# Kernel tuning notes

Hardware: AMD Instinct MI355X
Metric: run time of the kernel (lower is better)

## Reference

```python
import jax, jax.numpy as jnp
import numpy as np

B, S, HID, H, DK = 16, 1024, 512, 8, 64
NEG = -1e30


def setup_inputs() -> dict:
    key = jax.random.key(0)
    kx, kl, kq, kk, kv, ko = jax.random.split(key, 6)
    x = jax.random.normal(kx, (B, S, HID), dtype=jnp.float32)
    # mask is a prefix of ones per sample (the torch code fills nmask[i, :nsum, :nsum])
    lengths = jax.random.randint(kl, (B,), S // 2, S + 1)
    mask = (jnp.arange(S)[None, :] < lengths[:, None]).astype(jnp.int32)
    scale = 0.02
    Wq = jax.random.normal(kq, (H, HID, DK), dtype=jnp.float32) * scale  # stacked per-head Linear weights
    Wk = jax.random.normal(kk, (H, HID, DK), dtype=jnp.float32) * scale
    Wv = jax.random.normal(kv, (H, HID, DK), dtype=jnp.float32) * scale
    Wout = jax.random.normal(ko, (H * DK, HID), dtype=jnp.float32) * scale
    return {"x": x, "mask": mask, "Wq": Wq, "Wk": Wk, "Wv": Wv, "Wout": Wout}


def reference(x, mask, Wq, Wk, Wv, Wout):
    # x: [B,S,HID], mask: [B,S] int prefix mask
    nsum = mask.sum(-1).astype(jnp.float32)          # [B]
    valid = mask.astype(bool)                         # [B,S]
    pair = valid[:, :, None] & valid[:, None, :]      # [B,S,S] == nmask from the torch loop
    # batched per-head projections (equivalent to the per-head Linear loop)
    Q = jnp.einsum('bsh,nhd->bnsd', x, Wq)            # [B,H,S,DK]
    K = jnp.einsum('bsh,nhd->bnsd', x, Wk)
    V = jnp.einsum('bsh,nhd->bnsd', x, Wv)
    scores = jnp.einsum('bnqd,bnkd->bnqk', Q, K)      # [B,H,S,S]
    scores = scores / jnp.sqrt(nsum)[:, None, None, None]  # per-sample sqrt(len) scale
    scores = jnp.where(pair[:, None, :, :], scores, NEG)   # masked_softmax: -1e30 at masked slots
    p = jax.nn.softmax(scores, axis=-1)
    attn = jnp.einsum('bnqk,bnkd->bnqd', p, V)        # [B,H,S,DK]
    h = attn.transpose(0, 2, 1, 3).reshape(B, S, H * DK)  # concat heads along feature dim
    return jnp.einsum('bsf,fh->bsh', h, Wout)         # W_out, no bias
```

## Files before the change

kernel.cpp:

```cpp
#include <hip/hip_runtime.h>
#include <math.h>

constexpr int CB = 16;
constexpr int CS = 1024;
constexpr int CHID = 512;
constexpr int CH = 8;
constexpr int CDK = 64;

typedef _Float16 f16;
typedef __attribute__((ext_vector_type(8))) _Float16 f16x8;
typedef __attribute__((ext_vector_type(4))) _Float16 f16x4;
typedef __attribute__((ext_vector_type(4))) float f32x4;

__device__ inline f32x4 mfma16(f16x8 a, f16x8 b, f32x4 c) {
  return __builtin_amdgcn_mfma_f32_16x16x32_f16(a, b, c, 0, 0, 0);
}

__global__ __launch_bounds__(256) void lengths_kernel(const int* __restrict__ mask,
                                                      int* __restrict__ lens,
                                                      float* __restrict__ Vsum) {
  const int b = blockIdx.x, t = threadIdx.x;
  const int g = b * 256 + t;
  Vsum[g * 2] = 0.f;
  Vsum[g * 2 + 1] = 0.f;
  __shared__ int red[256];
  int s = 0;
  for (int i = t; i < CS; i += 256) s += mask[b * CS + i];
  red[t] = s;
  __syncthreads();
  for (int off = 128; off > 0; off >>= 1) {
    if (t < off) red[t] += red[t + off];
    __syncthreads();
  }
  if (t == 0) lens[b] = red[0];
}

__global__ __launch_bounds__(256) void cast_x_kernel(const float4* __restrict__ x,
                                                     f16x4* __restrict__ xh) {
  const int idx = blockIdx.x * 256 + threadIdx.x;
  const float4 v = x[idx];
  f16x4 o;
  o[0] = (f16)v.x; o[1] = (f16)v.y; o[2] = (f16)v.z; o[3] = (f16)v.w;
  xh[idx] = o;
}

__global__ __launch_bounds__(256) void cast_w_kernel(const float* __restrict__ Wq,
                                                     const float* __restrict__ Wk,
                                                     const float* __restrict__ Wv,
                                                     const float* __restrict__ Wout,
                                                     f16* __restrict__ wtAll) {
  const int y = blockIdx.y, kb = blockIdx.x, t = threadIdx.x;
  const int k0 = kb * 64;
  const float* src;
  int ldsrc;
  f16* dst;
  if (y < 24) {
    const int which = y >> 3, h = y & 7;
    const float* W = (which == 0) ? Wq : (which == 1) ? Wk : Wv;
    src = W + (size_t)h * 32768 + (size_t)k0 * 64;
    ldsrc = 64;
    dst = wtAll + (size_t)which * 262144 + (size_t)h * 32768;
  } else {
    const int c = y - 24;
    src = Wout + (size_t)k0 * 512 + c * 64;
    ldsrc = 512;
    dst = wtAll + (size_t)3 * 262144 + (size_t)c * 64 * 512;
  }

  __shared__ float Ts[64][68];
  {
    const int kr = t >> 4, cg = (t & 15) * 4;
#pragma unroll
    for (int rr = 0; rr < 4; ++rr) {
      const float4 v = *(const float4*)&src[(size_t)(rr * 16 + kr) * ldsrc + cg];
      Ts[rr * 16 + kr][cg] = v.x;
      Ts[rr * 16 + kr][cg + 1] = v.y;
      Ts[rr * 16 + kr][cg + 2] = v.z;
      Ts[rr * 16 + kr][cg + 3] = v.w;
    }
  }
  __syncthreads();
  {
    const int n = t >> 2, seg = t & 3;
    f16x8 a, b;
#pragma unroll
    for (int j = 0; j < 8; ++j) {
      a[j] = (f16)Ts[seg * 16 + j][n];
      b[j] = (f16)Ts[seg * 16 + 8 + j][n];
    }
    f16* d = &dst[(size_t)n * 512 + k0 + seg * 16];
    *(f16x8*)d = a;
    *(f16x8*)(d + 8) = b;
  }
}

__global__ __launch_bounds__(256) void qkvf_kernel(
    const f16* __restrict__ xh, const f16* __restrict__ wtAll,
    const int* __restrict__ lens, f16* __restrict__ Qh, f16* __restrict__ Kh,
    f16* __restrict__ Vth, float* __restrict__ Vsum) {
  const int rt = blockIdx.x, ct = blockIdx.y;
  const int which = ct >> 2, hp = ct & 3;
  const f16* Wt = wtAll + (size_t)which * 262144 + (size_t)hp * 65536;
  const int row0 = rt * 128;
  const int b = row0 >> 10, s0 = row0 & 1023;
  const int h0 = hp * 2;
  const int t = threadIdx.x;
  const int w = t >> 6, lane = t & 63, quad = lane >> 4, lcol = lane & 15;
  const int wr = w >> 1, wc = w & 1;

  __shared__ union SM {
    struct { f16 Xs[128][40]; f16 Ws[128][40]; } a;
    f16 Ts[128][136];
  } sm;

  f32x4 acc[4][4];
#pragma unroll
  for (int i = 0; i < 4; ++i)
#pragma unroll
    for (int j = 0; j < 4; ++j) acc[i][j] = (f32x4){0.f, 0.f, 0.f, 0.f};

  f16x8 px[2], pw[2];
#pragma unroll
  for (int i = 0; i < 2; ++i) {
    const int c = t + 256 * i, r = c >> 2, sg = c & 3;
    px[i] = *(const f16x8*)&xh[(size_t)(row0 + r) * CHID + sg * 8];
    pw[i] = *(const f16x8*)&Wt[(size_t)r * CHID + sg * 8];
  }

  for (int k0 = 0; k0 < CHID; k0 += 32) {
    __syncthreads();
#pragma unroll
    for (int i = 0; i < 2; ++i) {
      const int c = t + 256 * i, r = c >> 2, sg = c & 3;
      *(f16x8*)&sm.a.Xs[r][sg * 8] = px[i];
      *(f16x8*)&sm.a.Ws[r][sg * 8] = pw[i];
    }
    __syncthreads();
    const int kn = (k0 + 32 < CHID) ? k0 + 32 : k0;
#pragma unroll
    for (int i = 0; i < 2; ++i) {
      const int c = t + 256 * i, r = c >> 2, sg = c & 3;
      px[i] = *(const f16x8*)&xh[(size_t)(row0 + r) * CHID + kn + sg * 8];
      pw[i] = *(const f16x8*)&Wt[(size_t)r * CHID + kn + sg * 8];
    }
    f16x8 af[4], bf[4];
#pragma unroll
    for (int i = 0; i < 4; ++i)
      af[i] = *(const f16x8*)&sm.a.Xs[wr * 64 + i * 16 + lcol][quad * 8];
#pragma unroll
    for (int j = 0; j < 4; ++j)
      bf[j] = *(const f16x8*)&sm.a.Ws[wc * 64 + j * 16 + lcol][quad * 8];
#pragma unroll
    for (int i = 0; i < 4; ++i)
#pragma unroll
      for (int j = 0; j < 4; ++j) acc[i][j] = mfma16(af[i], bf[j], acc[i][j]);
  }

  if (which == 2) {
#pragma unroll
    for (int j = 0; j < 4; ++j) {
      float ps = 0.f;
#pragma unroll
      for (int i = 0; i < 4; ++i)
#pragma unroll
        for (int rr = 0; rr < 4; ++rr) ps += acc[i][j][rr];
      ps += __shfl_xor(ps, 16);
      ps += __shfl_xor(ps, 32);
      if (quad == 0) {
        const int d128 = wc * 64 + j * 16 + lcol;
        const int h = h0 + (d128 >> 6), d = d128 & 63;
        atomicAdd(&Vsum[((size_t)b * CH + h) * CDK + d], ps);
      }
    }
    __syncthreads();
#pragma unroll
    for (int i = 0; i < 4; ++i)
#pragma unroll
      for (int j = 0; j < 4; ++j)
#pragma unroll
        for (int rr = 0; rr < 4; ++rr)
          sm.Ts[wc * 64 + j * 16 + lcol][wr * 64 + i * 16 + quad * 4 + rr] =
              (f16)acc[i][j][rr];
    __syncthreads();
    const int nl = t >> 1, half = t & 1;
    const int h = h0 + (nl >> 6), d = nl & 63;
    f16* dst = &Vth[(((size_t)b * CH + h) * CDK + d) * CS + s0 + half * 64];
#pragma unroll
    for (int c8 = 0; c8 < 8; ++c8)
      *(f16x8*)&dst[c8 * 8] = *(const f16x8*)&sm.Ts[nl][half * 64 + c8 * 8];
  } else {
    f16* O = (which == 0) ? Qh : Kh;
    const float qsc = (which == 0) ? rsqrtf((float)lens[b]) : 1.0f;
    const int h = h0 + wc;
#pragma unroll
    for (int i = 0; i < 4; ++i) {
#pragma unroll
      for (int rr = 0; rr < 4; ++rr) {
        const int s = s0 + wr * 64 + i * 16 + quad * 4 + rr;
        const size_t base = (((size_t)b * CH + h) * CS + s) * CDK;
#pragma unroll
        for (int j = 0; j < 4; ++j)
          O[base + j * 16 + lcol] = (f16)(acc[i][j][rr] * qsc);
      }
    }
  }
}

__global__ __launch_bounds__(256) void attn_kernel(
    const f16* __restrict__ Qh, const f16* __restrict__ Kh,
    const f16* __restrict__ Vth, const int* __restrict__ lens,
    const float* __restrict__ Vsum, f16* __restrict__ Hbh) {
  const int qt = blockIdx.x, h = blockIdx.y, b = blockIdx.z;
  const int n = lens[b];
  const int nt = (n + 63) >> 6;
  const int t = threadIdx.x, w = t >> 6, lane = t & 63, quad = lane >> 4,
            lcol = lane & 15;

  __shared__ f16 Ks[64][72];
  __shared__ f16 Vs[64][72];
  __shared__ f16 Pt[4][32][72];

  const size_t bh = ((size_t)b * CH + h) * CS;
  const size_t bhd = ((size_t)b * CH + h) * CDK;

  const int qbase = qt * 128 + w * 32;
  f16x8 qa[2][2];
#pragma unroll
  for (int set = 0; set < 2; ++set) {
    const size_t qr = bh + qbase + set * 16 + lcol;
    qa[set][0] = *(const f16x8*)&Qh[qr * CDK + quad * 8];
    qa[set][1] = *(const f16x8*)&Qh[qr * CDK + 32 + quad * 8];
  }

  f32x4 o[2][4];
#pragma unroll
  for (int set = 0; set < 2; ++set)
#pragma unroll
    for (int dt = 0; dt < 4; ++dt) o[set][dt] = (f32x4){0.f, 0.f, 0.f, 0.f};
  float lp[2][4] = {{0.f, 0.f, 0.f, 0.f}, {0.f, 0.f, 0.f, 0.f}};

  f16x8 pk[2], pv[2];
#pragma unroll
  for (int i = 0; i < 2; ++i) {
    const int c = t + 256 * i, r = c >> 3, sg = c & 7;
    pk[i] = *(const f16x8*)&Kh[(bh + r) * CDK + sg * 8];
    pv[i] = *(const f16x8*)&Vth[(bhd + r) * CS + sg * 8];
  }

  for (int kt = 0; kt < nt; ++kt) {
    __syncthreads();
#pragma unroll
    for (int i = 0; i < 2; ++i) {
      const int c = t + 256 * i, r = c >> 3, sg = c & 7;
      *(f16x8*)&Ks[r][sg * 8] = pk[i];
      *(f16x8*)&Vs[r][sg * 8] = pv[i];
    }
    __syncthreads();
    const int ktn = (kt + 1 < nt) ? kt + 1 : kt;
#pragma unroll
    for (int i = 0; i < 2; ++i) {
      const int c = t + 256 * i, r = c >> 3, sg = c & 7;
      pk[i] = *(const f16x8*)&Kh[(bh + ktn * 64 + r) * CDK + sg * 8];
      pv[i] = *(const f16x8*)&Vth[(bhd + r) * CS + ktn * 64 + sg * 8];
    }

#pragma unroll
    for (int set = 0; set < 2; ++set) {
      f32x4 st[4];
#pragma unroll
      for (int ct = 0; ct < 4; ++ct) {
        const f16x8 kb0 = *(const f16x8*)&Ks[ct * 16 + lcol][quad * 8];
        const f16x8 kb1 = *(const f16x8*)&Ks[ct * 16 + lcol][32 + quad * 8];
        st[ct] = mfma16(qa[set][0], kb0, (f32x4){0.f, 0.f, 0.f, 0.f});
        st[ct] = mfma16(qa[set][1], kb1, st[ct]);
      }
#pragma unroll
      for (int ct = 0; ct < 4; ++ct) {
        const bool kvld = (kt * 64 + ct * 16 + lcol) < n;
#pragma unroll
        for (int r = 0; r < 4; ++r) {
          float p = __expf(st[ct][r]);
          p = kvld ? p : 0.f;
          lp[set][r] += p;
          Pt[w][set * 16 + quad * 4 + r][ct * 16 + lcol] = (f16)p;
        }
      }
    }

    f16x8 pa[2][2];
#pragma unroll
    for (int set = 0; set < 2; ++set) {
      pa[set][0] = *(const f16x8*)&Pt[w][set * 16 + lcol][quad * 8];
      pa[set][1] = *(const f16x8*)&Pt[w][set * 16 + lcol][32 + quad * 8];
    }

#pragma unroll
    for (int dt = 0; dt < 4; ++dt) {
      const f16x8 vb0 = *(const f16x8*)&Vs[dt * 16 + lcol][quad * 8];
      const f16x8 vb1 = *(const f16x8*)&Vs[dt * 16 + lcol][32 + quad * 8];
#pragma unroll
      for (int set = 0; set < 2; ++set) {
        o[set][dt] = mfma16(pa[set][0], vb0, o[set][dt]);
        o[set][dt] = mfma16(pa[set][1], vb1, o[set][dt]);
      }
    }
  }

  float invl[2][4];
#pragma unroll
  for (int set = 0; set < 2; ++set)
#pragma unroll
    for (int r = 0; r < 4; ++r) {
      float v = lp[set][r];
      v += __shfl_xor(v, 1);
      v += __shfl_xor(v, 2);
      v += __shfl_xor(v, 4);
      v += __shfl_xor(v, 8);
      invl[set][r] = 1.0f / v;
    }

#pragma unroll
  for (int set = 0; set < 2; ++set)
#pragma unroll
    for (int dt = 0; dt < 4; ++dt)
#pragma unroll
      for (int r = 0; r < 4; ++r) {
        const int srow = qbase + set * 16 + quad * 4 + r;
        const int d = dt * 16 + lcol;
        const float val = (srow < n) ? o[set][dt][r] * invl[set][r]
                                     : Vsum[bhd + d] * (1.0f / 1024.0f);
        Hbh[((size_t)b * CS + srow) * (CH * CDK) + h * CDK + d] = (f16)val;
      }
}

__global__ __launch_bounds__(256) void outp_kernel(const f16* __restrict__ Hbh,
                                                   const f16* __restrict__ woutt,
                                                   float* __restrict__ out) {
  const int rt = blockIdx.x, ctile = blockIdx.y;
  const int row0 = rt * 128, col0 = ctile * 128;
  const f16* Wt = woutt + (size_t)col0 * CHID;
  const int t = threadIdx.x;
  const int w = t >> 6, lane = t & 63, quad = lane >> 4, lcol = lane & 15;
  const int wr = w >> 1, wc = w & 1;

  __shared__ f16 Hs[128][40];
  __shared__ f16 Ws[128][40];

  f32x4 acc[4][4];
#pragma unroll
  for (int i = 0; i < 4; ++i)
#pragma unroll
    for (int j = 0; j < 4; ++j) acc[i][j] = (f32x4){0.f, 0.f, 0.f, 0.f};

  f16x8 ph[2], pw[2];
#pragma unroll
  for (int i = 0; i < 2; ++i) {
    const int c = t + 256 * i, r = c >> 2, sg = c & 3;
    ph[i] = *(const f16x8*)&Hbh[(size_t)(row0 + r) * CHID + sg * 8];
    pw[i] = *(const f16x8*)&Wt[(size_t)r * CHID + sg * 8];
  }

  for (int k0 = 0; k0 < CHID; k0 += 32) {
    __syncthreads();
#pragma unroll
    for (int i = 0; i < 2; ++i) {
      const int c = t + 256 * i, r = c >> 2, sg = c & 3;
      *(f16x8*)&Hs[r][sg * 8] = ph[i];
      *(f16x8*)&Ws[r][sg * 8] = pw[i];
    }
    __syncthreads();
    const int kn = (k0 + 32 < CHID) ? k0 + 32 : k0;
#pragma unroll
    for (int i = 0; i < 2; ++i) {
      const int c = t + 256 * i, r = c >> 2, sg = c & 3;
      ph[i] = *(const f16x8*)&Hbh[(size_t)(row0 + r) * CHID + kn + sg * 8];
      pw[i] = *(const f16x8*)&Wt[(size_t)r * CHID + kn + sg * 8];
    }
    f16x8 af[4], bf[4];
#pragma unroll
    for (int i = 0; i < 4; ++i)
      af[i] = *(const f16x8*)&Hs[wr * 64 + i * 16 + lcol][quad * 8];
#pragma unroll
    for (int j = 0; j < 4; ++j)
      bf[j] = *(const f16x8*)&Ws[wc * 64 + j * 16 + lcol][quad * 8];
#pragma unroll
    for (int i = 0; i < 4; ++i)
#pragma unroll
      for (int j = 0; j < 4; ++j) acc[i][j] = mfma16(af[i], bf[j], acc[i][j]);
  }

#pragma unroll
  for (int i = 0; i < 4; ++i) {
#pragma unroll
    for (int rr = 0; rr < 4; ++rr) {
      const size_t rg = row0 + wr * 64 + i * 16 + quad * 4 + rr;
#pragma unroll
      for (int j = 0; j < 4; ++j)
        out[rg * CHID + col0 + wc * 64 + j * 16 + lcol] = acc[i][j][rr];
    }
  }
}

extern "C" void kernel_launch(void* const* d_in, const int* in_sizes, int n_in,
                              void* d_out, int out_size, void* d_ws,
                              size_t ws_size, hipStream_t stream) {
  const float* x = (const float*)d_in[0];
  const int* mask = (const int*)d_in[1];
  const float* Wq = (const float*)d_in[2];
  const float* Wk = (const float*)d_in[3];
  const float* Wv = (const float*)d_in[4];
  const float* Wout = (const float*)d_in[5];
  float* out = (float*)d_out;

  char* ws = (char*)d_ws;
  int* lens = (int*)ws;
  size_t off = 1024;
  const size_t NX = (size_t)CB * CS * CHID;
  const size_t NW = (size_t)CH * CHID * CDK;
  f16* xh = (f16*)(ws + off);    off += NX * 2;
  f16* wtAll = (f16*)(ws + off); off += NW * 4 * 2;
  f16* Qh = (f16*)(ws + off);    off += NX * 2;
  f16* Kh = (f16*)(ws + off);    off += NX * 2;
  f16* Vth = (f16*)(ws + off);   off += NX * 2;
  f16* Hbh = (f16*)(ws + off);   off += NX * 2;
  float* Vsum = (float*)(ws + off); off += (size_t)CB * CH * CDK * 4;
  f16* woutt = wtAll + NW * 3;

  lengths_kernel<<<CB, 256, 0, stream>>>(mask, lens, Vsum);
  cast_x_kernel<<<NX / 4 / 256, 256, 0, stream>>>((const float4*)x, (f16x4*)xh);
  cast_w_kernel<<<dim3(8, 32), 256, 0, stream>>>(Wq, Wk, Wv, Wout, wtAll);
  qkvf_kernel<<<dim3(128, 12), 256, 0, stream>>>(xh, wtAll, lens, Qh, Kh, Vth,
                                                 Vsum);
  attn_kernel<<<dim3(CS / 128, CH, CB), 256, 0, stream>>>(Qh, Kh, Vth, lens,
                                                          Vsum, Hbh);
  outp_kernel<<<dim3(128, 4), 256, 0, stream>>>(Hbh, woutt, out);
}
```

Before: 213.5 us.

## Fuse prep kernels, coalesce stores via LDS, skip fully masked query tiles

Merges the length-reduction and x-cast kernels into one launch, and swaps the qkvf grid order so blocks sharing an x row tile run together. Q/K and attention-output stores are staged through shared memory and written as 16-byte vectors instead of scattered scalar stores. Attention blocks whose whole query tile lies past the valid length now write the mean-V fill directly and return early. The log2(e) factor is folded into the Q scale so the kernel can use exp2f, and K fragments are loaded once per tile instead of once per row set. The extra LDS staging adds barriers and some shared-memory traffic.

```diff
diff --git a/kernel.cpp b/kernel.cpp
--- a/kernel.cpp
+++ b/kernel.cpp
@@ -16,32 +16,36 @@
   return __builtin_amdgcn_mfma_f32_16x16x32_f16(a, b, c, 0, 0, 0);
 }
 
-__global__ __launch_bounds__(256) void lengths_kernel(const int* __restrict__ mask,
-                                                      int* __restrict__ lens,
-                                                      float* __restrict__ Vsum) {
-  const int b = blockIdx.x, t = threadIdx.x;
-  const int g = b * 256 + t;
-  Vsum[g * 2] = 0.f;
-  Vsum[g * 2 + 1] = 0.f;
+#define LOG2E 1.4426950408889634f
+
+__global__ __launch_bounds__(256) void prep_kernel(const float4* __restrict__ x,
+                                                   f16x4* __restrict__ xh,
+                                                   const int* __restrict__ mask,
+                                                   int* __restrict__ lens,
+                                                   float* __restrict__ Vsum) {
+  const int bid = blockIdx.x, t = threadIdx.x;
   __shared__ int red[256];
-  int s = 0;
-  for (int i = t; i < CS; i += 256) s += mask[b * CS + i];
-  red[t] = s;
-  __syncthreads();
-  for (int off = 128; off > 0; off >>= 1) {
-    if (t < off) red[t] += red[t + off];
-    __syncthreads();
-  }
-  if (t == 0) lens[b] = red[0];
-}
-
-__global__ __launch_bounds__(256) void cast_x_kernel(const float4* __restrict__ x,
-                                                     f16x4* __restrict__ xh) {
-  const int idx = blockIdx.x * 256 + threadIdx.x;
-  const float4 v = x[idx];
-  f16x4 o;
-  o[0] = (f16)v.x; o[1] = (f16)v.y; o[2] = (f16)v.z; o[3] = (f16)v.w;
-  xh[idx] = o;
+  if (bid < 8192) {
+    const int idx = bid * 256 + t;
+    const float4 v = x[idx];
+    f16x4 o;
+    o[0] = (f16)v.x; o[1] = (f16)v.y; o[2] = (f16)v.z; o[3] = (f16)v.w;
+    xh[idx] = o;
+  } else {
+    const int b = bid - 8192;
+    const int g = b * 256 + t;
+    Vsum[g * 2] = 0.f;
+    Vsum[g * 2 + 1] = 0.f;
+    int s = 0;
+    for (int i = t; i < CS; i += 256) s += mask[b * CS + i];
+    red[t] = s;
+    __syncthreads();
+    for (int off = 128; off > 0; off >>= 1) {
+      if (t < off) red[t] += red[t + off];
+      __syncthreads();
+    }
+    if (t == 0) lens[b] = red[0];
+  }
 }
 
 __global__ __launch_bounds__(256) void cast_w_kernel(const float* __restrict__ Wq,
@@ -98,7 +102,7 @@
     const f16* __restrict__ xh, const f16* __restrict__ wtAll,
     const int* __restrict__ lens, f16* __restrict__ Qh, f16* __restrict__ Kh,
     f16* __restrict__ Vth, float* __restrict__ Vsum) {
-  const int rt = blockIdx.x, ct = blockIdx.y;
+  const int ct = blockIdx.x, rt = blockIdx.y;
   const int which = ct >> 2, hp = ct & 3;
   const f16* Wt = wtAll + (size_t)which * 262144 + (size_t)hp * 65536;
   const int row0 = rt * 128;
@@ -176,31 +180,45 @@
 #pragma unroll
     for (int i = 0; i < 4; ++i)
 #pragma unroll
+      for (int j = 0; j < 4; ++j) {
+        f16x4 v4;
+#pragma unroll
+        for (int rr = 0; rr < 4; ++rr) v4[rr] = (f16)acc[i][j][rr];
+        *(f16x4*)&sm.Ts[wc * 64 + j * 16 + lcol][wr * 64 + i * 16 + quad * 4] =
+            v4;
+      }
+    __syncthreads();
+    const int c16 = t & 15;
+#pragma unroll
+    for (int p = 0; p < 8; ++p) {
+      const int vr = p * 16 + (t >> 4);
+      const int h = h0 + (vr >> 6), d = vr & 63;
+      *(f16x8*)&Vth[(((size_t)b * CH + h) * CDK + d) * CS + s0 + c16 * 8] =
+          *(const f16x8*)&sm.Ts[vr][c16 * 8];
+    }
+  } else {
+    const float qsc =
+        (which == 0) ? rsqrtf((float)lens[b]) * LOG2E : 1.0f;
+    __syncthreads();
+#pragma unroll
+    for (int i = 0; i < 4; ++i)
+#pragma unroll
       for (int j = 0; j < 4; ++j)
 #pragma unroll
         for (int rr = 0; rr < 4; ++rr)
-          sm.Ts[wc * 64 + j * 16 + lcol][wr * 64 + i * 16 + quad * 4 + rr] =
-              (f16)acc[i][j][rr];
-    __syncthreads();
-    const int nl = t >> 1, half = t & 1;
-    const int h = h0 + (nl >> 6), d = nl & 63;
-    f16* dst = &Vth[(((size_t)b * CH + h) * CDK + d) * CS + s0 + half * 64];
-#pragma unroll
-    for (int c8 = 0; c8 < 8; ++c8)
-      *(f16x8*)&dst[c8 * 8] = *(const f16x8*)&sm.Ts[nl][half * 64 + c8 * 8];
-  } else {
+          sm.Ts[wr * 64 + i * 16 + quad * 4 + rr][wc * 64 + j * 16 + lcol] =
+              (f16)(acc[i][j][rr] * qsc);
+    __syncthreads();
     f16* O = (which == 0) ? Qh : Kh;
-    const float qsc = (which == 0) ? rsqrtf((float)lens[b]) : 1.0f;
-    const int h = h0 + wc;
-#pragma unroll
-    for (int i = 0; i < 4; ++i) {
-#pragma unroll
-      for (int rr = 0; rr < 4; ++rr) {
-        const int s = s0 + wr * 64 + i * 16 + quad * 4 + rr;
-        const size_t base = (((size_t)b * CH + h) * CS + s) * CDK;
-#pragma unroll
-        for (int j = 0; j < 4; ++j)
-          O[base + j * 16 + lcol] = (f16)(acc[i][j][rr] * qsc);
+    const int c8 = t & 7;
+#pragma unroll
+    for (int p = 0; p < 4; ++p) {
+      const int row = p * 32 + (t >> 3);
+#pragma unroll
+      for (int half = 0; half < 2; ++half) {
+        const int h = h0 + half;
+        *(f16x8*)&O[(((size_t)b * CH + h) * CS + s0 + row) * CDK + c8 * 8] =
+            *(const f16x8*)&sm.Ts[row][half * 64 + c8 * 8];
       }
     }
   }
@@ -212,16 +230,32 @@
     const float* __restrict__ Vsum, f16* __restrict__ Hbh) {
   const int qt = blockIdx.x, h = blockIdx.y, b = blockIdx.z;
   const int n = lens[b];
-  const int nt = (n + 63) >> 6;
   const int t = threadIdx.x, w = t >> 6, lane = t & 63, quad = lane >> 4,
             lcol = lane & 15;
+
+  const size_t bh = ((size_t)b * CH + h) * CS;
+  const size_t bhd = ((size_t)b * CH + h) * CDK;
+
+  if (qt * 128 >= n) {
+    const int lr = lane >> 3, lc = lane & 7;
+    f16x8 mv;
+#pragma unroll
+    for (int j = 0; j < 8; ++j)
+      mv[j] = (f16)(Vsum[bhd + lc * 8 + j] * (1.0f / 1024.0f));
+#pragma unroll
+    for (int p = 0; p < 4; ++p) {
+      const int srow = qt * 128 + w * 32 + p * 8 + lr;
+      *(f16x8*)&Hbh[((size_t)b * CS + srow) * (CH * CDK) + h * CDK + lc * 8] =
+          mv;
+    }
+    return;
+  }
+
+  const int nt = (n + 63) >> 6;
 
   __shared__ f16 Ks[64][72];
   __shared__ f16 Vs[64][72];
   __shared__ f16 Pt[4][32][72];
-
-  const size_t bh = ((size_t)b * CH + h) * CS;
-  const size_t bhd = ((size_t)b * CH + h) * CDK;
 
   const int qbase = qt * 128 + w * 32;
   f16x8 qa[2][2];
@@ -264,22 +298,27 @@
       pv[i] = *(const f16x8*)&Vth[(bhd + r) * CS + ktn * 64 + sg * 8];
     }
 
+    f16x8 kb[4][2];
+#pragma unroll
+    for (int ct = 0; ct < 4; ++ct) {
+      kb[ct][0] = *(const f16x8*)&Ks[ct * 16 + lcol][quad * 8];
+      kb[ct][1] = *(const f16x8*)&Ks[ct * 16 + lcol][32 + quad * 8];
+    }
+
 #pragma unroll
     for (int set = 0; set < 2; ++set) {
       f32x4 st[4];
 #pragma unroll
       for (int ct = 0; ct < 4; ++ct) {
-        const f16x8 kb0 = *(const f16x8*)&Ks[ct * 16 + lcol][quad * 8];
-        const f16x8 kb1 = *(const f16x8*)&Ks[ct * 16 + lcol][32 + quad * 8];
-        st[ct] = mfma16(qa[set][0], kb0, (f32x4){0.f, 0.f, 0.f, 0.f});
-        st[ct] = mfma16(qa[set][1], kb1, st[ct]);
+        st[ct] = mfma16(qa[set][0], kb[ct][0], (f32x4){0.f, 0.f, 0.f, 0.f});
+        st[ct] = mfma16(qa[set][1], kb[ct][1], st[ct]);
       }
 #pragma unroll
       for (int ct = 0; ct < 4; ++ct) {
         const bool kvld = (kt * 64 + ct * 16 + lcol) < n;
 #pragma unroll
         for (int r = 0; r < 4; ++r) {
-          float p = __expf(st[ct][r]);
+          float p = exp2f(st[ct][r]);
           p = kvld ? p : 0.f;
           lp[set][r] += p;
           Pt[w][set * 16 + quad * 4 + r][ct * 16 + lcol] = (f16)p;
@@ -325,12 +364,22 @@
     for (int dt = 0; dt < 4; ++dt)
 #pragma unroll
       for (int r = 0; r < 4; ++r) {
-        const int srow = qbase + set * 16 + quad * 4 + r;
+        const int srow_l = set * 16 + quad * 4 + r;
         const int d = dt * 16 + lcol;
-        const float val = (srow < n) ? o[set][dt][r] * invl[set][r]
-                                     : Vsum[bhd + d] * (1.0f / 1024.0f);
-        Hbh[((size_t)b * CS + srow) * (CH * CDK) + h * CDK + d] = (f16)val;
-      }
+        const float val = (qbase + srow_l < n)
+                              ? o[set][dt][r] * invl[set][r]
+                              : Vsum[bhd + d] * (1.0f / 1024.0f);
+        Pt[w][srow_l][d] = (f16)val;
+      }
+  {
+    const int lr = lane >> 3, lc = lane & 7;
+#pragma unroll
+    for (int p = 0; p < 4; ++p) {
+      const int row = p * 8 + lr;
+      *(f16x8*)&Hbh[((size_t)b * CS + qbase + row) * (CH * CDK) + h * CDK +
+                    lc * 8] = *(const f16x8*)&Pt[w][row][lc * 8];
+    }
+  }
 }
 
 __global__ __launch_bounds__(256) void outp_kernel(const f16* __restrict__ Hbh,
@@ -426,10 +475,10 @@
   float* Vsum = (float*)(ws + off); off += (size_t)CB * CH * CDK * 4;
   f16* woutt = wtAll + NW * 3;
 
-  lengths_kernel<<<CB, 256, 0, stream>>>(mask, lens, Vsum);
-  cast_x_kernel<<<NX / 4 / 256, 256, 0, stream>>>((const float4*)x, (f16x4*)xh);
+  prep_kernel<<<8208, 256, 0, stream>>>((const float4*)x, (f16x4*)xh, mask,
+                                        lens, Vsum);
   cast_w_kernel<<<dim3(8, 32), 256, 0, stream>>>(Wq, Wk, Wv, Wout, wtAll);
-  qkvf_kernel<<<dim3(128, 12), 256, 0, stream>>>(xh, wtAll, lens, Qh, Kh, Vth,
+  qkvf_kernel<<<dim3(12, 128), 256, 0, stream>>>(xh, wtAll, lens, Qh, Kh, Vth,
                                                  Vsum);
   attn_kernel<<<dim3(CS / 128, CH, CB), 256, 0, stream>>>(Qh, Kh, Vth, lens,
                                                           Vsum, Hbh);
```

After: 226.3 us. 1.06x slower.
